# Optimization experiments

Hardware: AMD Instinct MI355X
Metric: run time of the kernel (lower is better)

The kernel has to match this reference:

```python
import jax, jax.numpy as jnp
import numpy as np

N, E = 20000, 320000          # nodes, edges (avg in-degree ~16)
F_IN, EMB, T, OUT = 40, 40, 5, 2
F_T = EMB // T                # per-tower output width = 8
EPS_STD, EPS_GN = 1e-5, 1e-5


def _lin_init(k, fan_in, fan_out, extra=()):
    return jax.random.normal(k, (*extra, fan_in, fan_out), jnp.float32) / np.sqrt(fan_in)


def setup_inputs() -> dict:
    key = jax.random.key(0)
    ks = jax.random.split(key, 8)
    # deg histogram in init: all 20000 nodes with degree 16 -> avg_deg['log'] = log(16+1)
    return dict(
        x=jax.random.normal(ks[0], (N, F_IN), jnp.float32),
        edge_index=jax.random.randint(ks[1], (2, E), 0, N),
        W_pre=_lin_init(ks[2], 2 * F_IN, F_IN, (T,)),   # per-tower pre-MLP
        b_pre=jnp.zeros((T, F_IN), jnp.float32),
        W_post=_lin_init(ks[3], 13 * F_IN, F_T, (T,)),  # (4 agg * 3 scalers + 1 residual) * F_in
        b_post=jnp.zeros((T, F_T), jnp.float32),
        W_lin=_lin_init(ks[4], T * F_T, EMB),           # PNAConv final mixing linear
        b_lin=jnp.zeros((EMB,), jnp.float32),
        gn_weight=jnp.ones((EMB,), jnp.float32),
        gn_bias=jnp.zeros((EMB,), jnp.float32),
        gn_mean_scale=jnp.ones((EMB,), jnp.float32),
        W1=_lin_init(ks[5], EMB, EMB),                  # head hidden linear
        b1=jnp.zeros((EMB,), jnp.float32),
        W2=_lin_init(ks[6], EMB, OUT),                  # head output linear
        b2=jnp.zeros((OUT,), jnp.float32),
        avg_deg_log=jnp.float32(np.log(17.0)),
    )


def _pna_conv(x, src, dst, W_pre, b_pre, W_post, b_post, W_lin, b_lin, avg_deg_log):
    xi, xj = x[dst], x[src]                              # gather: [E, F]
    h = jnp.concatenate([xi, xj], axis=-1)               # [E, 2F]
    m = jnp.einsum('ef,tfg->etg', h, W_pre) + b_pre      # per-tower messages [E, T, F]
    cnt = jax.ops.segment_sum(jnp.ones((E,), m.dtype), dst, num_segments=N)  # in-degree [N]
    denom = jnp.maximum(cnt, 1.0)[:, None, None]
    mean = jax.ops.segment_sum(m, dst, num_segments=N) / denom
    mean2 = jax.ops.segment_sum(m * m, dst, num_segments=N) / denom
    std = jnp.sqrt(jax.nn.relu(mean2 - mean * mean) + EPS_STD)
    has = (cnt > 0)[:, None, None]
    mn = jnp.where(has, jax.ops.segment_min(m, dst, num_segments=N), 0.0)
    mx = jnp.where(has, jax.ops.segment_max(m, dst, num_segments=N), 0.0)
    agg = jnp.concatenate([mean, mn, mx, std], axis=-1)  # [N, T, 4F]
    deg = jnp.maximum(cnt, 1.0)[:, None, None]
    logd = jnp.log(deg + 1.0)
    out = jnp.concatenate(
        [agg, agg * (logd / avg_deg_log), agg * (avg_deg_log / logd)], axis=-1)  # [N, T, 12F]
    out = jnp.concatenate(
        [jnp.broadcast_to(x[:, None, :], (N, T, x.shape[-1])), out], axis=-1)    # [N, T, 13F]
    out = jnp.einsum('ntf,tfg->ntg', out, W_post) + b_post                       # [N, T, F_T]
    return out.reshape(N, T * F_T) @ W_lin + b_lin


def _graph_norm(x, w, b, mean_scale):
    mean = jnp.mean(x, axis=0, keepdims=True)
    out = x - mean_scale * mean
    var = jnp.mean(out * out, axis=0, keepdims=True)
    return w * out / jnp.sqrt(var + EPS_GN) + b


def reference(x, edge_index, W_pre, b_pre, W_post, b_post, W_lin, b_lin,
              gn_weight, gn_bias, gn_mean_scale, W1, b1, W2, b2, avg_deg_log):
    src, dst = edge_index[0], edge_index[1]
    h = _pna_conv(x, src, dst, W_pre, b_pre, W_post, b_post, W_lin, b_lin, avg_deg_log)
    h = jax.nn.relu(_graph_norm(h, gn_weight, gn_bias, gn_mean_scale))
    h = jax.nn.relu(h @ W1 + b1)   # dropout_rate=None -> no dropout
    return h @ W2 + b2
```

## Files before the change

### kernel.cpp

```cpp
#include <hip/hip_runtime.h>
#include <math.h>

#define N_NODES 20000
#define N_EDGES 320000
#define F_IN 40
#define T_TOW 5
#define EMB 40
#define NPB_PRE 16
#define NBLK_MIX 313
#define NBLK_PM 625
#define ECHUNK 16
#define STRIDE 64
#define CPAD 16

typedef __attribute__((ext_vector_type(8))) _Float16 half8;
typedef __attribute__((ext_vector_type(2))) _Float16 half2_t;
typedef __attribute__((ext_vector_type(4))) float f32x4;

#define WS_STATS   0
#define WS_CURSOR  320
#define WS_SSRC    1280384
#define WS_MS      6400384
#define WS_MD      14400384
#define WS_AGG     22400384
#define WS_XPOST   54400384
#define WS_H0T     57600384
#define WS_PART    60800384

__global__ __launch_bounds__(256) void k_pre(const float* __restrict__ x,
                                             const float* __restrict__ W_pre,
                                             const float* __restrict__ b_pre,
                                             const float* __restrict__ W_post,
                                             const float* __restrict__ b_post,
                                             _Float16* __restrict__ mS,
                                             _Float16* __restrict__ mD,
                                             float* __restrict__ xpostT,
                                             int* __restrict__ cursor) {
  const int tid = threadIdx.x;
  const int n0 = blockIdx.x * NPB_PRE;
  if (tid < NPB_PRE) cursor[(n0 + tid) * CPAD] = (n0 + tid) * STRIDE;
  const bool statlane = tid < 200;
  const int q = tid - 200;
  const bool xplane = (q >= 0 && q < 40);
  const int tc = statlane ? tid : 199;
  const int t = tc / 40, g = tc - t * 40;
  const int t2 = xplane ? q / 8 : 0, g2 = xplane ? q - (q / 8) * 8 : 0;
  float wA[40], wB[40];
  const float* Wt = W_pre + t * 3200;
#pragma unroll
  for (int j = 0; j < 40; ++j) {
    wA[j] = statlane ? Wt[j * 40 + g] : W_post[t2 * 4160 + j * 8 + g2];
    wB[j] = statlane ? Wt[(40 + j) * 40 + g] : 0.f;
  }
  const float bias = statlane ? b_pre[t * 40 + g] : b_post[t2 * 8 + g2];
  for (int ni = 0; ni < NPB_PRE; ++ni) {
    const int n = n0 + ni;
    const float* xr = x + n * F_IN;
    float aA = bias, aB = 0.f;
#pragma unroll
    for (int j = 0; j < 40; j += 4) {
      const float4 xv = *(const float4*)(xr + j);
      aA += xv.x * wA[j] + xv.y * wA[j + 1] + xv.z * wA[j + 2] + xv.w * wA[j + 3];
      aB += xv.x * wB[j] + xv.y * wB[j + 1] + xv.z * wB[j + 2] + xv.w * wB[j + 3];
    }
    if (statlane) {
      mD[n * 200 + tc] = (_Float16)aA;
      mS[n * 200 + tc] = (_Float16)aB;
    } else if (xplane) {
      xpostT[t2 * (N_NODES * 8) + n * 8 + g2] = aA;
    }
  }
}

__global__ __launch_bounds__(256) void k_scatter(const int* __restrict__ src,
                                                 const int* __restrict__ dst,
                                                 int* __restrict__ cursor,
                                                 int* __restrict__ ssrc) {
  int i = blockIdx.x * 256 + threadIdx.x;
  if (i < N_EDGES) {
    int d = dst[i];
    int pos = atomicAdd(&cursor[d * CPAD], 1);
    ssrc[pos] = src[i];
  }
}

__global__ __launch_bounds__(256) void k_edge(const _Float16* __restrict__ mS,
                                              const _Float16* __restrict__ mD,
                                              const int* __restrict__ cursor,
                                              const int* __restrict__ ssrc,
                                              _Float16* __restrict__ aggS) {
  const int lane = threadIdx.x & 63;
  const int wv = threadIdx.x >> 6;
  const int n = blockIdx.x * 4 + wv;
  const int r0 = n * STRIDE;
  const int r1 = __builtin_amdgcn_readfirstlane(cursor[n * CPAD]);
  const int cnt = r1 - r0;
  const int myidx = ssrc[r0 + lane];
  const int cpa = lane;
  const bool bact = lane < 36;
  const int cpb = bact ? 64 + lane : 99;
  const half2_t mda = ((const half2_t*)(mD + n * 200))[cpa];
  const half2_t mdb = ((const half2_t*)(mD + n * 200))[cpb];

  const _Float16 HINF = (_Float16)65504.f;
  half2_t suma = {0, 0}, ssqa = {0, 0}, sumb = {0, 0}, ssqb = {0, 0};
  half2_t mna = {HINF, HINF}, mxa = {-HINF, -HINF};
  half2_t mnb = {HINF, HINF}, mxb = {-HINF, -HINF};
  half2_t va = {0, 0}, vb = {0, 0};

  if (cnt > 0) {
    for (int p = 0; p < cnt; p += ECHUNK) {
      half2_t ha[ECHUNK], hb[ECHUNK];
#pragma unroll
      for (int i = 0; i < ECHUNK; ++i) {
        const int ii = (p + i < cnt) ? (p + i) : (cnt - 1);
        const int s = __builtin_amdgcn_readlane(myidx, ii);
        const half2_t* row = (const half2_t*)(mS + s * 200);
        ha[i] = row[cpa];
        hb[i] = row[cpb];
      }
#pragma unroll
      for (int i = 0; i < ECHUNK; ++i) {
        suma += ha[i];
        ssqa += ha[i] * ha[i];
        mna = __builtin_elementwise_min(mna, ha[i]);
        mxa = __builtin_elementwise_max(mxa, ha[i]);
        sumb += hb[i];
        ssqb += hb[i] * hb[i];
        mnb = __builtin_elementwise_min(mnb, hb[i]);
        mxb = __builtin_elementwise_max(mxb, hb[i]);
      }
      va = ha[ECHUNK - 1];
      vb = hb[ECHUNK - 1];
    }
  }

  const int padded = ((cnt + ECHUNK - 1) / ECHUNK) * ECHUNK;
  const float d = (float)(padded - cnt);
  const float inv = (cnt > 0) ? 1.f / (float)cnt : 0.f;
#pragma unroll
  for (int set = 0; set < 2; ++set) {
    if (set == 1 && !bact) break;
    const int cp = set == 0 ? cpa : cpb;
    const half2_t sum2 = set == 0 ? suma : sumb;
    const half2_t ssq2 = set == 0 ? ssqa : ssqb;
    const half2_t mn2 = set == 0 ? mna : mnb;
    const half2_t mx2 = set == 0 ? mxa : mxb;
    const half2_t vl2 = set == 0 ? va : vb;
    const half2_t md2 = set == 0 ? mda : mdb;
    half2_t omean, omn, omx, osd;
#pragma unroll
    for (int j = 0; j < 2; ++j) {
      float mean, mnf, mxf, sd;
      if (cnt > 0) {
        const float vl = (float)vl2[j];
        const float sf = (float)sum2[j] - d * vl;
        const float qf = (float)ssq2[j] - d * vl * vl;
        const float msm = sf * inv;
        const float var = qf * inv - msm * msm;
        sd = sqrtf(fmaxf(var, 0.f) + 1e-5f);
        const float mdf = (float)md2[j];
        mean = mdf + msm;
        mnf = mdf + (float)mn2[j];
        mxf = mdf + (float)mx2[j];
      } else {
        mean = 0.f; mnf = 0.f; mxf = 0.f; sd = sqrtf(1e-5f);
      }
      omean[j] = (_Float16)mean;
      omn[j] = (_Float16)mnf;
      omx[j] = (_Float16)mxf;
      osd[j] = (_Float16)sd;
    }
    const int t = cp / 20, g = 2 * (cp - t * 20);
    _Float16* abase = aggS + ((size_t)t * N_NODES + n) * 160 + g;
    *(half2_t*)(abase) = omean;
    *(half2_t*)(abase + 40) = omn;
    *(half2_t*)(abase + 80) = omx;
    *(half2_t*)(abase + 120) = osd;
  }
}

__global__ __launch_bounds__(320) void k_postmix(const _Float16* __restrict__ aggT,
                                                 const int* __restrict__ cursor,
                                                 const float* __restrict__ W_post,
                                                 const float* __restrict__ avg_dl,
                                                 const float* __restrict__ xpostT,
                                                 const float* __restrict__ W_lin,
                                                 const float* __restrict__ b_lin,
                                                 float* __restrict__ h0T,
                                                 float* __restrict__ partial) {
  __shared__ float sP[32 * 41];
  const int tid = threadIdx.x;
  const int t = tid >> 6;
  const int l = tid & 63;
  const int n0 = blockIdx.x * 32;
  const int c = l & 15;
  const int kg = l >> 4;

  const float* Wt = W_post + t * 4160;
  half8 b1f[5], b2f[5];
#pragma unroll
  for (int ks = 0; ks < 5; ++ks) {
#pragma unroll
    for (int j = 0; j < 8; ++j) {
      const int k = ks * 32 + kg * 8 + j;
      const float w1v = (c < 8) ? Wt[(40 + k) * 8 + c] : Wt[(200 + k) * 8 + (c - 8)];
      const float w2v = (c < 8) ? Wt[(360 + k) * 8 + c] : 0.f;
      b1f[ks][j] = (_Float16)w1v;
      b2f[ks][j] = (_Float16)w2v;
    }
  }
  const float avg = avg_dl[0];

  for (int tile = 0; tile < 2; ++tile) {
    const int nb = n0 + tile * 16;
    const int nA = nb + c;
    const half8* ar = (const half8*)(aggT + ((size_t)t * N_NODES + nA) * 160);
    half8 af[5];
#pragma unroll
    for (int ks = 0; ks < 5; ++ks) af[ks] = ar[ks * 4 + kg];
    f32x4 acc1 = {0.f, 0.f, 0.f, 0.f}, acc2 = {0.f, 0.f, 0.f, 0.f};
#pragma unroll
    for (int ks = 0; ks < 5; ++ks) {
      acc1 = __builtin_amdgcn_mfma_f32_16x16x32_f16(af[ks], b1f[ks], acc1, 0, 0, 0);
      acc2 = __builtin_amdgcn_mfma_f32_16x16x32_f16(af[ks], b2f[ks], acc2, 0, 0, 0);
    }
    float bp[4];
#pragma unroll
    for (int r = 0; r < 4; ++r) bp[r] = __shfl_xor(acc1[r], 8, 64);
    if (c < 8) {
#pragma unroll
      for (int r = 0; r < 4; ++r) {
        const int nn = nb + kg * 4 + r;
        const int cnt = cursor[nn * CPAD] - nn * STRIDE;
        const float ld = logf(fmaxf((float)cnt, 1.f) + 1.f);
        const float s1 = ld / avg, s2 = avg / ld;
        const float xp = xpostT[t * (N_NODES * 8) + nn * 8 + c];
        sP[(tile * 16 + kg * 4 + r) * 41 + t * 8 + c] =
            acc1[r] + s1 * bp[r] + s2 * acc2[r] + xp;
      }
    }
  }
  __syncthreads();

  const int nb = l & 31;
  const int ch = l >> 5;
  const int cc = t * 8 + ch * 4;
  const float4 bb = *(const float4*)(b_lin + cc);
  float acc[4] = {bb.x, bb.y, bb.z, bb.w};
  for (int k = 0; k < 40; ++k) {
    const float p = sP[nb * 41 + k];
    const float4 w = *(const float4*)(W_lin + k * EMB + cc);
    acc[0] = fmaf(p, w.x, acc[0]);
    acc[1] = fmaf(p, w.y, acc[1]);
    acc[2] = fmaf(p, w.z, acc[2]);
    acc[3] = fmaf(p, w.w, acc[3]);
  }
  const int n = n0 + nb;
#pragma unroll
  for (int j = 0; j < 4; ++j) h0T[(cc + j) * N_NODES + n] = acc[j];
#pragma unroll
  for (int j = 0; j < 4; ++j) {
    float sv = acc[j];
    float qv = acc[j] * acc[j];
#pragma unroll
    for (int m = 1; m <= 16; m <<= 1) {
      sv += __shfl_xor(sv, m, 64);
      qv += __shfl_xor(qv, m, 64);
    }
    if (nb == 0) {
      partial[blockIdx.x * 80 + cc + j] = sv;
      partial[blockIdx.x * 80 + 40 + cc + j] = qv;
    }
  }
}

__global__ __launch_bounds__(256) void k_stats(const float* __restrict__ partial,
                                               float* __restrict__ S1,
                                               float* __restrict__ S2) {
  const int col = blockIdx.x;
  const int tid = threadIdx.x;
  __shared__ float red[4];
  float s = 0.f;
  for (int b = tid; b < NBLK_PM; b += 256) s += partial[b * 80 + col];
#pragma unroll
  for (int m = 32; m >= 1; m >>= 1) s += __shfl_xor(s, m, 64);
  if ((tid & 63) == 0) red[tid >> 6] = s;
  __syncthreads();
  if (tid == 0) {
    const float tot = (red[0] + red[1]) + (red[2] + red[3]);
    if (col < 40) S1[col] = tot;
    else S2[col - 40] = tot;
  }
}

__global__ __launch_bounds__(256) void k_head(const float* __restrict__ S1,
                                              const float* __restrict__ S2,
                                              const float* __restrict__ h0T,
                                              const float* __restrict__ gn_w,
                                              const float* __restrict__ gn_b,
                                              const float* __restrict__ gn_ms,
                                              const float* __restrict__ W1,
                                              const float* __restrict__ b1,
                                              const float* __restrict__ W2,
                                              const float* __restrict__ b2,
                                              float* __restrict__ out) {
  __shared__ float sV[64 * 41];
  __shared__ float sH[64 * 41];
  const int tid = threadIdx.x;
  const int n0 = blockIdx.x * 64;
  const float invN = 1.f / (float)N_NODES;
  for (int i = 0; i < 10; ++i) {
    const int idx = tid + i * 256;
    const int e = idx >> 6, r = idx & 63;
    const int nn0 = n0 + r;
    const int nn = (nn0 < N_NODES) ? nn0 : 0;
    const float M = S1[e] * invN;
    const float ms = gn_ms[e];
    const float var = S2[e] * invN - ms * (2.f - ms) * M * M;
    const float sc = gn_w[e] / sqrtf(var + 1e-5f);
    const float he = h0T[e * N_NODES + nn];
    sV[r * 41 + e] = fmaxf((he - ms * M) * sc + gn_b[e], 0.f);
  }
  __syncthreads();
  const int wv = tid >> 6, lane = tid & 63;
  const int c0 = wv * 10;
  float acc[10];
#pragma unroll
  for (int j = 0; j < 10; ++j) acc[j] = b1[c0 + j];
  for (int k = 0; k < 40; ++k) {
    const float p = sV[lane * 41 + k];
    const float* w = W1 + k * EMB + c0;
#pragma unroll
    for (int j = 0; j < 10; ++j) acc[j] = fmaf(p, w[j], acc[j]);
  }
#pragma unroll
  for (int j = 0; j < 10; ++j) sH[lane * 41 + c0 + j] = fmaxf(acc[j], 0.f);
  __syncthreads();
  if (tid < 64) {
    const int n = n0 + tid;
    if (n < N_NODES) {
      float o0 = b2[0], o1 = b2[1];
      const float* hr = sH + tid * 41;
#pragma unroll
      for (int k = 0; k < 40; ++k) {
        const float r = hr[k];
        o0 = fmaf(r, W2[k * 2], o0);
        o1 = fmaf(r, W2[k * 2 + 1], o1);
      }
      out[n * 2] = o0;
      out[n * 2 + 1] = o1;
    }
  }
}

extern "C" void kernel_launch(void* const* d_in, const int* in_sizes, int n_in,
                              void* d_out, int out_size, void* d_ws, size_t ws_size,
                              hipStream_t stream) {
  const float* x      = (const float*)d_in[0];
  const int*   ei     = (const int*)d_in[1];
  const float* W_pre  = (const float*)d_in[2];
  const float* b_pre  = (const float*)d_in[3];
  const float* W_post = (const float*)d_in[4];
  const float* b_post = (const float*)d_in[5];
  const float* W_lin  = (const float*)d_in[6];
  const float* b_lin  = (const float*)d_in[7];
  const float* gn_w   = (const float*)d_in[8];
  const float* gn_b   = (const float*)d_in[9];
  const float* gn_ms  = (const float*)d_in[10];
  const float* W1     = (const float*)d_in[11];
  const float* b1     = (const float*)d_in[12];
  const float* W2     = (const float*)d_in[13];
  const float* b2     = (const float*)d_in[14];
  const float* avg_dl = (const float*)d_in[15];
  float* out = (float*)d_out;

  char* ws = (char*)d_ws;
  float* S1   = (float*)(ws + WS_STATS);
  float* S2   = S1 + 40;
  int* cursor = (int*)(ws + WS_CURSOR);
  int* ssrc   = (int*)(ws + WS_SSRC);
  _Float16* mS   = (_Float16*)(ws + WS_MS);
  _Float16* mD   = (_Float16*)(ws + WS_MD);
  _Float16* aggS = (_Float16*)(ws + WS_AGG);
  float* xpostT  = (float*)(ws + WS_XPOST);
  float* h0T     = (float*)(ws + WS_H0T);
  float* part    = (float*)(ws + WS_PART);
  const int* e_src = ei;
  const int* e_dst = ei + N_EDGES;

  k_pre<<<N_NODES / NPB_PRE, 256, 0, stream>>>(x, W_pre, b_pre, W_post, b_post,
                                               mS, mD, xpostT, cursor);
  k_scatter<<<(N_EDGES + 255) / 256, 256, 0, stream>>>(e_src, e_dst, cursor, ssrc);
  k_edge<<<N_NODES / 4, 256, 0, stream>>>(mS, mD, cursor, ssrc, aggS);
  k_postmix<<<NBLK_PM, 320, 0, stream>>>(aggS, cursor, W_post, avg_dl,
                                         xpostT, W_lin, b_lin, h0T, part);
  k_stats<<<80, 256, 0, stream>>>(part, S1, S2);
  k_head<<<NBLK_MIX, 256, 0, stream>>>(S1, S2, h0T, gn_w, gn_b, gn_ms,
                                       W1, b1, W2, b2, out);
}
```

Baseline: 195.5 us.

## Precompute postmix weight fragments in k_pre and fold stats reduction into k_head

Extra blocks in k_pre convert the W_post slices to fp16 MFMA fragment layout once and store them in workspace. k_postmix then loads ready-made half8 fragments instead of doing strided fp32 gathers and conversions in every block. The separate k_stats launch is removed. Each k_head block now re-reduces the 625x80 partial sums itself, which saves one kernel launch but repeats that reduction across 313 blocks.

New measurement: 193.4 us. Within noise of the previous version (-1.1%).

```diff
diff --git a/kernel.cpp b/kernel.cpp
--- a/kernel.cpp
+++ b/kernel.cpp
@@ -7,6 +7,7 @@
 #define T_TOW 5
 #define EMB 40
 #define NPB_PRE 16
+#define NBLK_PRE 1250
 #define NBLK_MIX 313
 #define NBLK_PM 625
 #define ECHUNK 16
@@ -17,7 +18,6 @@
 typedef __attribute__((ext_vector_type(2))) _Float16 half2_t;
 typedef __attribute__((ext_vector_type(4))) float f32x4;
 
-#define WS_STATS   0
 #define WS_CURSOR  320
 #define WS_SSRC    1280384
 #define WS_MS      6400384
@@ -26,6 +26,8 @@
 #define WS_XPOST   54400384
 #define WS_H0T     57600384
 #define WS_PART    60800384
+#define WS_FRAG1   61000384
+#define WS_FRAG2   61026048
 
 __global__ __launch_bounds__(256) void k_pre(const float* __restrict__ x,
                                              const float* __restrict__ W_pre,
@@ -35,8 +37,30 @@
                                              _Float16* __restrict__ mS,
                                              _Float16* __restrict__ mD,
                                              float* __restrict__ xpostT,
-                                             int* __restrict__ cursor) {
+                                             int* __restrict__ cursor,
+                                             _Float16* __restrict__ frag1,
+                                             _Float16* __restrict__ frag2) {
   const int tid = threadIdx.x;
+  if (blockIdx.x >= NBLK_PRE) {
+    const int bid2 = blockIdx.x - NBLK_PRE;
+    if (tid < 64) {
+      const int t = bid2 / 5, ks = bid2 - (bid2 / 5) * 5;
+      const int c = tid & 15, kg = tid >> 4;
+      const float* Wt = W_post + t * 4160;
+      half8 v1, v2;
+#pragma unroll
+      for (int j = 0; j < 8; ++j) {
+        const int k = ks * 32 + kg * 8 + j;
+        const float w1v = (c < 8) ? Wt[(40 + k) * 8 + c] : Wt[(200 + k) * 8 + (c - 8)];
+        const float w2v = (c < 8) ? Wt[(360 + k) * 8 + c] : 0.f;
+        v1[j] = (_Float16)w1v;
+        v2[j] = (_Float16)w2v;
+      }
+      ((half8*)frag1)[(t * 5 + ks) * 64 + tid] = v1;
+      ((half8*)frag2)[(t * 5 + ks) * 64 + tid] = v2;
+    }
+    return;
+  }
   const int n0 = blockIdx.x * NPB_PRE;
   if (tid < NPB_PRE) cursor[(n0 + tid) * CPAD] = (n0 + tid) * STRIDE;
   const bool statlane = tid < 200;
@@ -182,7 +206,8 @@
 
 __global__ __launch_bounds__(320) void k_postmix(const _Float16* __restrict__ aggT,
                                                  const int* __restrict__ cursor,
-                                                 const float* __restrict__ W_post,
+                                                 const _Float16* __restrict__ frag1,
+                                                 const _Float16* __restrict__ frag2,
                                                  const float* __restrict__ avg_dl,
                                                  const float* __restrict__ xpostT,
                                                  const float* __restrict__ W_lin,
@@ -197,18 +222,13 @@
   const int c = l & 15;
   const int kg = l >> 4;
 
-  const float* Wt = W_post + t * 4160;
+  const half8* f1 = (const half8*)frag1 + t * 320 + l;
+  const half8* f2 = (const half8*)frag2 + t * 320 + l;
   half8 b1f[5], b2f[5];
 #pragma unroll
   for (int ks = 0; ks < 5; ++ks) {
-#pragma unroll
-    for (int j = 0; j < 8; ++j) {
-      const int k = ks * 32 + kg * 8 + j;
-      const float w1v = (c < 8) ? Wt[(40 + k) * 8 + c] : Wt[(200 + k) * 8 + (c - 8)];
-      const float w2v = (c < 8) ? Wt[(360 + k) * 8 + c] : 0.f;
-      b1f[ks][j] = (_Float16)w1v;
-      b2f[ks][j] = (_Float16)w2v;
-    }
+    b1f[ks] = f1[ks * 64];
+    b2f[ks] = f2[ks * 64];
   }
   const float avg = avg_dl[0];
 
@@ -275,27 +295,7 @@
   }
 }
 
-__global__ __launch_bounds__(256) void k_stats(const float* __restrict__ partial,
-                                               float* __restrict__ S1,
-                                               float* __restrict__ S2) {
-  const int col = blockIdx.x;
-  const int tid = threadIdx.x;
-  __shared__ float red[4];
-  float s = 0.f;
-  for (int b = tid; b < NBLK_PM; b += 256) s += partial[b * 80 + col];
-#pragma unroll
-  for (int m = 32; m >= 1; m >>= 1) s += __shfl_xor(s, m, 64);
-  if ((tid & 63) == 0) red[tid >> 6] = s;
-  __syncthreads();
-  if (tid == 0) {
-    const float tot = (red[0] + red[1]) + (red[2] + red[3]);
-    if (col < 40) S1[col] = tot;
-    else S2[col - 40] = tot;
-  }
-}
-
-__global__ __launch_bounds__(256) void k_head(const float* __restrict__ S1,
-                                              const float* __restrict__ S2,
+__global__ __launch_bounds__(256) void k_head(const float* __restrict__ partial,
                                               const float* __restrict__ h0T,
                                               const float* __restrict__ gn_w,
                                               const float* __restrict__ gn_b,
@@ -307,17 +307,37 @@
                                               float* __restrict__ out) {
   __shared__ float sV[64 * 41];
   __shared__ float sH[64 * 41];
+  __shared__ float sSp[3][80];
   const int tid = threadIdx.x;
   const int n0 = blockIdx.x * 64;
   const float invN = 1.f / (float)N_NODES;
+  if (tid < 240) {
+    const int chunk = tid / 80;
+    const int col = tid - chunk * 80;
+    const int b0 = chunk * 209;
+    const int b1e = (b0 + 209 < NBLK_PM) ? b0 + 209 : NBLK_PM;
+    float a0 = 0.f, a1 = 0.f, a2 = 0.f, a3 = 0.f;
+    int b = b0;
+    for (; b + 4 <= b1e; b += 4) {
+      a0 += partial[(b + 0) * 80 + col];
+      a1 += partial[(b + 1) * 80 + col];
+      a2 += partial[(b + 2) * 80 + col];
+      a3 += partial[(b + 3) * 80 + col];
+    }
+    for (; b < b1e; ++b) a0 += partial[b * 80 + col];
+    sSp[chunk][col] = (a0 + a1) + (a2 + a3);
+  }
+  __syncthreads();
   for (int i = 0; i < 10; ++i) {
     const int idx = tid + i * 256;
     const int e = idx >> 6, r = idx & 63;
     const int nn0 = n0 + r;
     const int nn = (nn0 < N_NODES) ? nn0 : 0;
-    const float M = S1[e] * invN;
+    const float S1e = sSp[0][e] + sSp[1][e] + sSp[2][e];
+    const float S2e = sSp[0][40 + e] + sSp[1][40 + e] + sSp[2][40 + e];
+    const float M = S1e * invN;
     const float ms = gn_ms[e];
-    const float var = S2[e] * invN - ms * (2.f - ms) * M * M;
+    const float var = S2e * invN - ms * (2.f - ms) * M * M;
     const float sc = gn_w[e] / sqrtf(var + 1e-5f);
     const float he = h0T[e * N_NODES + nn];
     sV[r * 41 + e] = fmaxf((he - ms * M) * sc + gn_b[e], 0.f);
@@ -376,8 +396,6 @@
   float* out = (float*)d_out;
 
   char* ws = (char*)d_ws;
-  float* S1   = (float*)(ws + WS_STATS);
-  float* S2   = S1 + 40;
   int* cursor = (int*)(ws + WS_CURSOR);
   int* ssrc   = (int*)(ws + WS_SSRC);
   _Float16* mS   = (_Float16*)(ws + WS_MS);
@@ -386,16 +404,17 @@
   float* xpostT  = (float*)(ws + WS_XPOST);
   float* h0T     = (float*)(ws + WS_H0T);
   float* part    = (float*)(ws + WS_PART);
+  _Float16* frag1 = (_Float16*)(ws + WS_FRAG1);
+  _Float16* frag2 = (_Float16*)(ws + WS_FRAG2);
   const int* e_src = ei;
   const int* e_dst = ei + N_EDGES;
 
-  k_pre<<<N_NODES / NPB_PRE, 256, 0, stream>>>(x, W_pre, b_pre, W_post, b_post,
-                                               mS, mD, xpostT, cursor);
+  k_pre<<<NBLK_PRE + 25, 256, 0, stream>>>(x, W_pre, b_pre, W_post, b_post,
+                                           mS, mD, xpostT, cursor, frag1, frag2);
   k_scatter<<<(N_EDGES + 255) / 256, 256, 0, stream>>>(e_src, e_dst, cursor, ssrc);
   k_edge<<<N_NODES / 4, 256, 0, stream>>>(mS, mD, cursor, ssrc, aggS);
-  k_postmix<<<NBLK_PM, 320, 0, stream>>>(aggS, cursor, W_post, avg_dl,
+  k_postmix<<<NBLK_PM, 320, 0, stream>>>(aggS, cursor, frag1, frag2, avg_dl,
                                          xpostT, W_lin, b_lin, h0T, part);
-  k_stats<<<80, 256, 0, stream>>>(part, S1, S2);
-  k_head<<<NBLK_MIX, 256, 0, stream>>>(S1, S2, h0T, gn_w, gn_b, gn_ms,
+  k_head<<<NBLK_MIX, 256, 0, stream>>>(part, h0T, gn_w, gn_b, gn_ms,
                                        W1, b1, W2, b2, out);
 }
```
